# Optimization experiments

Hardware: AMD Instinct MI355X
Metric: run time of the kernel (lower is better)

Reference implementation:

```python
import jax, jax.numpy as jnp
import numpy as np
import math

H = 5       # attention heads
DK = 20     # attdim // H
ATT = 100   # attdim
LAYERS = 2
B, L, BERT_DIM = 32, 256, 768


def _layernorm(x, a, b, eps=1e-6):
    mean = x.mean(-1, keepdims=True)
    std = jnp.std(x, axis=-1, ddof=1, keepdims=True)  # torch.std is unbiased
    return a * (x - mean) / (std + eps) + b


def _forward(sequence_output, src_mask, aspect_mask, short_mask,
             ln_a, ln_b, Wxx_w, Wxx_b, q_w, q_b, k_w, k_b,
             dense_w, dense_b, bias_m, W_w, W_b, Wx_w, Wx_b, clf_w, clf_b):
    Bn, Ln, _ = sequence_output.shape
    x = _layernorm(sequence_output, ln_a, ln_b)
    g = x @ Wxx_w + Wxx_b                                  # [B,L,100]
    asp_wn = aspect_mask.sum(1, keepdims=True)             # [B,1]
    aspect = (g * aspect_mask[..., None]).sum(1) / asp_wn  # [B,100]

    q = (g @ q_w + q_b).reshape(Bn, Ln, H, DK).transpose(0, 2, 1, 3)  # [B,H,L,dk]
    k = (g @ k_w + k_b).reshape(Bn, Ln, H, DK).transpose(0, 2, 1, 3)
    # aspect is expanded identically across heads/positions before dense -> [B,dk]
    asp = aspect @ dense_w + dense_b                       # [B,dk]
    scores = jnp.einsum('bhid,bhjd->bhij', q, k) / math.sqrt(DK)
    asp_sc = jnp.tanh(jnp.einsum('bd,bhjd->bhj', asp, k) + bias_m[0])
    scores = scores + asp_sc[:, :, None, :]
    scores = jnp.where(src_mask[:, None, None, :] == 0, -1e9, scores)
    scores = scores + short_mask                           # [B,1,L,L] broadcast
    adj = jax.nn.softmax(scores, axis=-1)                  # [B,H,L,L]

    # edge-update linear split so the [B,L,L,205] concat is never materialized:
    # edge[b,i,j] = adj_perm[b,i,j] @ Wa + go[b,j] @ W1 + go[b,i] @ W2 + b
    Wa, W1, W2 = Wx_w[:H], Wx_w[H:H + ATT], Wx_w[H + ATT:]
    go = g
    for i in range(LAYERS):
        # expand+matmul+mean over heads == mean-head message passing
        Ax = jnp.einsum('bhij,bjd->bid', adj, go) / H
        go = jax.nn.relu(Ax @ W_w + W_b)
        if i < LAYERS - 1:  # last edge update is discarded by the original output
            edge = (jnp.einsum('bhij,hk->bijk', adj, Wa)
                    + (go @ W1)[:, None, :, :]
                    + (go @ W2)[:, :, None, :]
                    + Wx_b)
            adj = edge.transpose(0, 3, 1, 2)
    # original: node_outputs = F.relu(gcn_outputs) (aggregate_W result is overwritten)
    h = jax.nn.relu(go)
    out1 = (h * aspect_mask[..., None]).sum(1) / asp_wn    # [B,100]
    return out1 @ clf_w + clf_b                            # [B,3]


def setup_inputs() -> dict:
    key = jax.random.key(0)
    ks = jax.random.split(key, 24)
    f32 = jnp.float32
    p = lambda k, shape, s=0.05: jax.random.normal(k, shape, dtype=f32) * s
    src_mask = jax.random.randint(ks[0], (B, L), 0, 2, dtype=jnp.int32).at[:, 0].set(1)
    aspect_mask = jnp.zeros((B, L), f32).at[:, 4:8].set(1.0)  # aspect span tokens
    return {
        'sequence_output': jax.random.normal(ks[1], (B, L, BERT_DIM), dtype=f32),
        'src_mask': src_mask,
        'aspect_mask': aspect_mask,
        'short_mask': p(ks[2], (B, 1, L, L), 1.0),
        'ln_a': jnp.ones((BERT_DIM,), f32),
        'ln_b': jnp.zeros((BERT_DIM,), f32),
        'Wxx_w': p(ks[3], (BERT_DIM, ATT)), 'Wxx_b': p(ks[4], (ATT,)),
        'q_w': p(ks[5], (ATT, ATT)), 'q_b': p(ks[6], (ATT,)),
        'k_w': p(ks[7], (ATT, ATT)), 'k_b': p(ks[8], (ATT,)),
        'dense_w': p(ks[9], (ATT, DK)), 'dense_b': p(ks[10], (DK,)),
        'bias_m': p(ks[11], (1,)),
        'W_w': p(ks[12], (ATT, ATT)), 'W_b': p(ks[13], (ATT,)),
        'Wx_w': p(ks[14], (H + 2 * ATT, H)), 'Wx_b': p(ks[15], (H,)),
        'clf_w': p(ks[16], (ATT, 3)), 'clf_b': p(ks[17], (3,)),
    }


def reference(sequence_output, src_mask, aspect_mask, short_mask,
              ln_a, ln_b, Wxx_w, Wxx_b, q_w, q_b, k_w, k_b,
              dense_w, dense_b, bias_m, W_w, W_b, Wx_w, Wx_b, clf_w, clf_b):
    return _forward(sequence_output, src_mask, aspect_mask, short_mask,
                    ln_a, ln_b, Wxx_w, Wxx_b, q_w, q_b, k_w, k_b,
                    dense_w, dense_b, bias_m, W_w, W_b, Wx_w, Wx_b, clf_w, clf_b)
```

## Files before the change

### kernel.cpp

```cpp
#include <hip/hip_runtime.h>
#include <math.h>

constexpr int CL = 256;
constexpr int CD = 768;
constexpr int CATT = 100;
constexpr int CH = 5;
constexpr int CDK = 20;

__device__ __forceinline__ void fma4(float4& a, float s, const float4& w) {
    a.x = fmaf(s, w.x, a.x);
    a.y = fmaf(s, w.y, a.y);
    a.z = fmaf(s, w.z, a.z);
    a.w = fmaf(s, w.w, a.w);
}

__global__ __launch_bounds__(256) void k1_fused(
    const float* __restrict__ x, const float* __restrict__ ln_a,
    const float* __restrict__ ln_b, const float* __restrict__ Wxx_w,
    const float* __restrict__ Wxx_b, const float* __restrict__ q_w,
    const float* __restrict__ q_b, const float* __restrict__ k_w,
    const float* __restrict__ k_b, const float* __restrict__ amask,
    float* __restrict__ g, float* __restrict__ qt, float* __restrict__ ktb,
    float* __restrict__ aspect_raw)
{
    __shared__ float s_mean[16], s_rinv[16];
    __shared__ float s_xn[16 * 68];
    __shared__ float s_w[100 * 104];
    __shared__ float s_gt[16 * 100];

    const int t = threadIdx.x;
    const int r0 = blockIdx.x * 16;
    const int wid = t >> 6, lane = t & 63;

    for (int rr = wid * 4; rr < wid * 4 + 4; ++rr) {
        const float* xr = x + (size_t)(r0 + rr) * CD;
        float xv[12];
        float s = 0.f;
#pragma unroll
        for (int m = 0; m < 12; ++m) { xv[m] = xr[lane + 64 * m]; s += xv[m]; }
#pragma unroll
        for (int o = 32; o; o >>= 1) s += __shfl_xor(s, o);
        float mean = s * (1.0f / 768.0f);
        float sq = 0.f;
#pragma unroll
        for (int m = 0; m < 12; ++m) { float d = xv[m] - mean; sq = fmaf(d, d, sq); }
#pragma unroll
        for (int o = 32; o; o >>= 1) sq += __shfl_xor(sq, o);
        if (lane == 0) {
            s_mean[rr] = mean;
            s_rinv[rr] = 1.0f / (sqrtf(sq * (1.0f / 767.0f)) + 1e-6f);
        }
    }
    __syncthreads();

    const int cg = t % 25, rg = t / 25;
    const int c = cg * 4;
    float4 acc0 = make_float4(0.f, 0.f, 0.f, 0.f);
    float4 acc1 = make_float4(0.f, 0.f, 0.f, 0.f);

    for (int kt = 0; kt < 12; ++kt) {
#pragma unroll
        for (int m = 0; m < 4; ++m) {
            int idx = t + 256 * m;
            int row = idx >> 6, kk = idx & 63;
            int k = kt * 64 + kk;
            float v = x[(size_t)(r0 + row) * CD + k];
            s_xn[row * 68 + kk] = fmaf(ln_a[k], (v - s_mean[row]) * s_rinv[row], ln_b[k]);
        }
        const float4* wsrc = (const float4*)Wxx_w + (size_t)kt * 1600;
        for (int i = t; i < 1600; i += 256) {
            int row = i / 25, c4 = i % 25;
            *(float4*)&s_w[row * 104 + c4 * 4] = wsrc[i];
        }
        __syncthreads();
        if (t < 200) {
#pragma unroll 2
            for (int kk = 0; kk < 64; kk += 4) {
                float4 a0 = *(const float4*)&s_xn[(rg * 2 + 0) * 68 + kk];
                float4 a1 = *(const float4*)&s_xn[(rg * 2 + 1) * 68 + kk];
                float4 w0 = *(const float4*)&s_w[(kk + 0) * 104 + c];
                float4 w1 = *(const float4*)&s_w[(kk + 1) * 104 + c];
                float4 w2 = *(const float4*)&s_w[(kk + 2) * 104 + c];
                float4 w3 = *(const float4*)&s_w[(kk + 3) * 104 + c];
                fma4(acc0, a0.x, w0); fma4(acc0, a0.y, w1); fma4(acc0, a0.z, w2); fma4(acc0, a0.w, w3);
                fma4(acc1, a1.x, w0); fma4(acc1, a1.y, w1); fma4(acc1, a1.z, w2); fma4(acc1, a1.w, w3);
            }
        }
        __syncthreads();
    }
    if (t < 200) {
        float4 bias = *(const float4*)&Wxx_b[c];
        float4 rr0, rr1;
        rr0.x = acc0.x + bias.x; rr0.y = acc0.y + bias.y; rr0.z = acc0.z + bias.z; rr0.w = acc0.w + bias.w;
        rr1.x = acc1.x + bias.x; rr1.y = acc1.y + bias.y; rr1.z = acc1.z + bias.z; rr1.w = acc1.w + bias.w;
        float4 rv[2] = { rr0, rr1 };
#pragma unroll
        for (int q = 0; q < 2; ++q) {
            int row = r0 + rg * 2 + q;
            *(float4*)&g[(size_t)row * CATT + c] = rv[q];
            *(float4*)&s_gt[(rg * 2 + q) * 100 + c] = rv[q];
            float m = amask[row];
            if (m != 0.f) {
                int b = row >> 8;
                atomicAdd(&aspect_raw[b * CATT + c + 0], m * rv[q].x);
                atomicAdd(&aspect_raw[b * CATT + c + 1], m * rv[q].y);
                atomicAdd(&aspect_raw[b * CATT + c + 2], m * rv[q].z);
                atomicAdd(&aspect_raw[b * CATT + c + 3], m * rv[q].w);
            }
        }
    }
    __syncthreads();

    for (int pass = 0; pass < 2; ++pass) {
        const float4* ws4 = (const float4*)(pass ? k_w : q_w);
        for (int i = t; i < 2500; i += 256) {
            int row = i / 25, c4 = i % 25;
            *(float4*)&s_w[row * 104 + c4 * 4] = ws4[i];
        }
        __syncthreads();
        if (t < 200) {
            const float* bb = pass ? k_b : q_b;
            float* outp = pass ? ktb : qt;
            float4 b0 = make_float4(0.f, 0.f, 0.f, 0.f);
            float4 b1 = make_float4(0.f, 0.f, 0.f, 0.f);
#pragma unroll 2
            for (int k = 0; k < 100; k += 4) {
                float4 a0 = *(const float4*)&s_gt[(rg * 2 + 0) * 100 + k];
                float4 a1 = *(const float4*)&s_gt[(rg * 2 + 1) * 100 + k];
                float4 w0 = *(const float4*)&s_w[(k + 0) * 104 + c];
                float4 w1 = *(const float4*)&s_w[(k + 1) * 104 + c];
                float4 w2 = *(const float4*)&s_w[(k + 2) * 104 + c];
                float4 w3 = *(const float4*)&s_w[(k + 3) * 104 + c];
                fma4(b0, a0.x, w0); fma4(b0, a0.y, w1); fma4(b0, a0.z, w2); fma4(b0, a0.w, w3);
                fma4(b1, a1.x, w0); fma4(b1, a1.y, w1); fma4(b1, a1.z, w2); fma4(b1, a1.w, w3);
            }
            float4 bias = *(const float4*)&bb[c];
            b0.x += bias.x; b0.y += bias.y; b0.z += bias.z; b0.w += bias.w;
            b1.x += bias.x; b1.y += bias.y; b1.z += bias.z; b1.w += bias.w;
            const int h = c / CDK, d = c % CDK;
            float4 rv[2] = { b0, b1 };
#pragma unroll
            for (int q = 0; q < 2; ++q) {
                int row = r0 + rg * 2 + q;
                int bidx = row >> 8, l = row & 255;
                *(float4*)&outp[((size_t)(bidx * CH + h) * CL + l) * CDK + d] = rv[q];
            }
        }
        __syncthreads();
    }
}

__global__ __launch_bounds__(256) void k2_small(
    const float* __restrict__ aspect_raw, const float* __restrict__ amask,
    const float* __restrict__ dense_w, const float* __restrict__ dense_b,
    float* __restrict__ asp, float* __restrict__ aspwn)
{
    __shared__ float red[4];
    const int b = blockIdx.x, t = threadIdx.x;
    const int wid = t >> 6, lane = t & 63;
    float s = amask[b * CL + t];
#pragma unroll
    for (int o = 32; o; o >>= 1) s += __shfl_xor(s, o);
    if (lane == 0) red[wid] = s;
    __syncthreads();
    float wn = red[0] + red[1] + red[2] + red[3];
    if (t == 0) aspwn[b] = wn;
    if (t < 20) {
        float a = dense_b[t];
        float rwn = 1.f / wn;
        for (int d = 0; d < CATT; ++d)
            a = fmaf(aspect_raw[b * CATT + d] * rwn, dense_w[d * CDK + t], a);
        asp[b * CDK + t] = a;
    }
}

__global__ __launch_bounds__(256) void k45_attn_gcn0(
    const float* __restrict__ qt, const float* __restrict__ ktb,
    const float* __restrict__ asp, const float* __restrict__ bias_m,
    const int* __restrict__ src_mask, const float* __restrict__ shortm,
    const float* __restrict__ Wx_w, const float* __restrict__ g,
    const float* __restrict__ W_w, const float* __restrict__ W_b,
    float* __restrict__ adjW, float* __restrict__ go1,
    float* __restrict__ t1, float* __restrict__ t2, float* __restrict__ gW2S)
{
    constexpr int ICH = 16;
    __shared__ float s_adj[16 * 260];
    __shared__ float s_b[100 * 104];
    __shared__ float s_ax[16 * 108];
    __shared__ float s_q[ICH * CDK];
    __shared__ float s_red[ICH * 4];
    __shared__ float s_was[5];
    __shared__ float s_aspb[20];
    __shared__ float s_w1[100], s_w2[100];
    __shared__ float s_g1row[16];

    const int b = blockIdx.x >> 4, ic = blockIdx.x & 15;
    const int i0 = ic * 16;
    const int t = threadIdx.x, lane = t & 63, wid = t >> 6;
    const int j = t;

    if (t < 5) {
        float s = 0.f;
        for (int k2 = 0; k2 < 5; ++k2) s += Wx_w[t * 5 + k2];
        s_was[t] = s;
    }
    if (t < 20) s_aspb[t] = asp[b * CDK + t];
    if (t < 100) {
        float a = 0.f, c2 = 0.f;
#pragma unroll
        for (int h = 0; h < 5; ++h) {
            a += Wx_w[(5 + t) * 5 + h];
            c2 += Wx_w[(105 + t) * 5 + h];
        }
        s_w1[t] = a; s_w2[t] = c2;
    }

    const bool masked = (src_mask[b * CL + j] == 0);
    const float bm = bias_m[0];
    const float rs20 = 0.223606797749978969f;

    float sm[ICH];
#pragma unroll
    for (int ii = 0; ii < ICH; ++ii)
        sm[ii] = shortm[(size_t)(b * CL + i0 + ii) * CL + j];

    float accS[ICH], accW[ICH];
#pragma unroll
    for (int ii = 0; ii < ICH; ++ii) { accS[ii] = 0.f; accW[ii] = 0.f; }

    for (int h = 0; h < CH; ++h) {
        __syncthreads();
        {
            const size_t base = ((size_t)(b * CH + h) * CL + i0) * CDK;
            s_q[t] = qt[base + t];
            if (t < ICH * CDK - 256) s_q[256 + t] = qt[base + 256 + t];
        }
        float4 kr[5];
        const float* kp = ktb + ((size_t)(b * CH + h) * CL + j) * CDK;
#pragma unroll
        for (int m = 0; m < 5; ++m) kr[m] = *(const float4*)(kp + 4 * m);
        __syncthreads();

        const float was_h = s_was[h];
        float s = bm;
#pragma unroll
        for (int m = 0; m < 5; ++m) {
            s = fmaf(s_aspb[4 * m + 0], kr[m].x, s);
            s = fmaf(s_aspb[4 * m + 1], kr[m].y, s);
            s = fmaf(s_aspb[4 * m + 2], kr[m].z, s);
            s = fmaf(s_aspb[4 * m + 3], kr[m].w, s);
        }
        const float aspsc = tanhf(s);

        float pv[ICH];
#pragma unroll
        for (int ii = 0; ii < ICH; ++ii) {
            const float* qrow = &s_q[ii * CDK];
            float sc = 0.f;
#pragma unroll
            for (int m = 0; m < 5; ++m) {
                float4 q4 = *(const float4*)(qrow + 4 * m);
                sc = fmaf(q4.x, kr[m].x, sc);
                sc = fmaf(q4.y, kr[m].y, sc);
                sc = fmaf(q4.z, kr[m].z, sc);
                sc = fmaf(q4.w, kr[m].w, sc);
            }
            sc = fmaf(sc, rs20, aspsc) + sm[ii];
            float p = masked ? 0.f : __expf(sc);
            pv[ii] = p;
            float ssum = p;
#pragma unroll
            for (int o = 32; o; o >>= 1) ssum += __shfl_xor(ssum, o);
            if (lane == 0) s_red[ii * 4 + wid] = ssum;
        }
        __syncthreads();
#pragma unroll
        for (int ii = 0; ii < ICH; ++ii) {
            float tot = s_red[ii * 4 + 0] + s_red[ii * 4 + 1] +
                        s_red[ii * 4 + 2] + s_red[ii * 4 + 3];
            float pn = pv[ii] * __frcp_rn(tot);
            accS[ii] += pn;
            accW[ii] = fmaf(was_h, pn, accW[ii]);
        }
    }

#pragma unroll
    for (int ii = 0; ii < ICH; ++ii) {
        adjW[(size_t)(b * CL + i0 + ii) * CL + j] = accW[ii];
        s_adj[ii * 260 + j] = accS[ii];
    }
    __syncthreads();

    const int cg = t % 25, rg = t / 25;
    const int c = cg * 4;
    float4 acc0 = make_float4(0.f, 0.f, 0.f, 0.f);
    float4 acc1 = make_float4(0.f, 0.f, 0.f, 0.f);
    for (int jt = 0; jt < 4; ++jt) {
        const float4* src = (const float4*)g + (size_t)(b * CL + jt * 64) * 25;
        for (int i = t; i < 1600; i += 256) {
            int row = i / 25, c4 = i % 25;
            *(float4*)&s_b[row * 104 + c4 * 4] = src[i];
        }
        __syncthreads();
        if (t < 200) {
#pragma unroll 2
            for (int kk = 0; kk < 64; kk += 4) {
                float4 a0 = *(const float4*)&s_adj[(rg * 2 + 0) * 260 + jt * 64 + kk];
                float4 a1 = *(const float4*)&s_adj[(rg * 2 + 1) * 260 + jt * 64 + kk];
                float4 w0 = *(const float4*)&s_b[(kk + 0) * 104 + c];
                float4 w1 = *(const float4*)&s_b[(kk + 1) * 104 + c];
                float4 w2 = *(const float4*)&s_b[(kk + 2) * 104 + c];
                float4 w3 = *(const float4*)&s_b[(kk + 3) * 104 + c];
                fma4(acc0, a0.x, w0); fma4(acc0, a0.y, w1); fma4(acc0, a0.z, w2); fma4(acc0, a0.w, w3);
                fma4(acc1, a1.x, w0); fma4(acc1, a1.y, w1); fma4(acc1, a1.z, w2); fma4(acc1, a1.w, w3);
            }
        }
        __syncthreads();
    }
    if (t < 200) {
        float4 r;
        r.x = acc0.x * 0.2f; r.y = acc0.y * 0.2f; r.z = acc0.z * 0.2f; r.w = acc0.w * 0.2f;
        *(float4*)&s_ax[(rg * 2 + 0) * 108 + c] = r;
        r.x = acc1.x * 0.2f; r.y = acc1.y * 0.2f; r.z = acc1.z * 0.2f; r.w = acc1.w * 0.2f;
        *(float4*)&s_ax[(rg * 2 + 1) * 108 + c] = r;
    }
    {
        const float4* ws4 = (const float4*)W_w;
        for (int i = t; i < 2500; i += 256) {
            int row = i / 25, c4 = i % 25;
            *(float4*)&s_b[row * 104 + c4 * 4] = ws4[i];
        }
    }
    __syncthreads();

    float4 o0 = make_float4(0.f, 0.f, 0.f, 0.f);
    float4 o1 = make_float4(0.f, 0.f, 0.f, 0.f);
    if (t < 200) {
#pragma unroll 2
        for (int k = 0; k < 100; k += 4) {
            float4 a0 = *(const float4*)&s_ax[(rg * 2 + 0) * 108 + k];
            float4 a1 = *(const float4*)&s_ax[(rg * 2 + 1) * 108 + k];
            float4 w0 = *(const float4*)&s_b[(k + 0) * 104 + c];
            float4 w1 = *(const float4*)&s_b[(k + 1) * 104 + c];
            float4 w2 = *(const float4*)&s_b[(k + 2) * 104 + c];
            float4 w3 = *(const float4*)&s_b[(k + 3) * 104 + c];
            fma4(o0, a0.x, w0); fma4(o0, a0.y, w1); fma4(o0, a0.z, w2); fma4(o0, a0.w, w3);
            fma4(o1, a1.x, w0); fma4(o1, a1.y, w1); fma4(o1, a1.z, w2); fma4(o1, a1.w, w3);
        }
        float4 bias = *(const float4*)&W_b[c];
        o0.x = fmaxf(o0.x + bias.x, 0.f); o0.y = fmaxf(o0.y + bias.y, 0.f);
        o0.z = fmaxf(o0.z + bias.z, 0.f); o0.w = fmaxf(o0.w + bias.w, 0.f);
        o1.x = fmaxf(o1.x + bias.x, 0.f); o1.y = fmaxf(o1.y + bias.y, 0.f);
        o1.z = fmaxf(o1.z + bias.z, 0.f); o1.w = fmaxf(o1.w + bias.w, 0.f);
        *(float4*)&go1[(size_t)(b * CL + i0 + rg * 2 + 0) * CATT + c] = o0;
        *(float4*)&go1[(size_t)(b * CL + i0 + rg * 2 + 1) * CATT + c] = o1;
    }
    __syncthreads();

    float* s_go = s_adj;
    if (t < 200) {
        *(float4*)&s_go[(rg * 2 + 0) * 104 + c] = o0;
        *(float4*)&s_go[(rg * 2 + 1) * 104 + c] = o1;
    }
    __syncthreads();

    if (t < 128) {
        int r = t >> 3, seg = t & 7;
        int e0 = seg * 13, e1 = e0 + 13 < 100 ? e0 + 13 : 100;
        float a = 0.f, c2 = 0.f;
        for (int e = e0; e < e1; ++e) {
            float v = s_go[r * 104 + e];
            a = fmaf(v, s_w1[e], a);
            c2 = fmaf(v, s_w2[e], c2);
        }
        a += __shfl_xor(a, 1); a += __shfl_xor(a, 2); a += __shfl_xor(a, 4);
        c2 += __shfl_xor(c2, 1); c2 += __shfl_xor(c2, 2); c2 += __shfl_xor(c2, 4);
        if (seg == 0) {
            s_g1row[r] = a;
            gW2S[b * CL + i0 + r] = c2;
        }
    }
    __syncthreads();

    if (t < 100) {
        float a = 0.f, s2 = 0.f;
#pragma unroll
        for (int r = 0; r < 16; ++r) {
            float v = s_go[r * 104 + t];
            a = fmaf(s_g1row[r], v, a);
            s2 += v;
        }
        atomicAdd(&t1[b * CATT + t], a);
        atomicAdd(&t2[b * CATT + t], s2);
    }
}

__global__ __launch_bounds__(256) void k7_gcn1(
    const float* __restrict__ adjW, const float* __restrict__ go1,
    const float* __restrict__ W_w, const float* __restrict__ W_b,
    const float* __restrict__ t1, const float* __restrict__ t2,
    const float* __restrict__ gW2S, const float* __restrict__ Wx_b,
    const float* __restrict__ amask, float* __restrict__ out1_raw)
{
    __shared__ float s_adj[16 * 260];
    __shared__ float s_b[100 * 104];
    __shared__ float s_ax[16 * 108];
    const int b = blockIdx.x >> 4, ic = blockIdx.x & 15;
    const int i0 = ic * 16;
    const int t = threadIdx.x;

    {
        const float4* asrc = (const float4*)adjW + (size_t)(b * CL + i0) * 64;
        for (int i = t; i < 1024; i += 256) {
            int row = i >> 6, c4 = i & 63;
            *(float4*)&s_adj[row * 260 + c4 * 4] = asrc[i];
        }
    }
    __syncthreads();

    const int cg = t % 25, rg = t / 25;
    const int c = cg * 4;
    float4 acc0 = make_float4(0.f, 0.f, 0.f, 0.f);
    float4 acc1 = make_float4(0.f, 0.f, 0.f, 0.f);
    for (int jt = 0; jt < 4; ++jt) {
        const float4* src = (const float4*)go1 + (size_t)(b * CL + jt * 64) * 25;
        for (int i = t; i < 1600; i += 256) {
            int row = i / 25, c4 = i % 25;
            *(float4*)&s_b[row * 104 + c4 * 4] = src[i];
        }
        __syncthreads();
        if (t < 200) {
#pragma unroll 2
            for (int kk = 0; kk < 64; kk += 4) {
                float4 a0 = *(const float4*)&s_adj[(rg * 2 + 0) * 260 + jt * 64 + kk];
                float4 a1 = *(const float4*)&s_adj[(rg * 2 + 1) * 260 + jt * 64 + kk];
                float4 w0 = *(const float4*)&s_b[(kk + 0) * 104 + c];
                float4 w1 = *(const float4*)&s_b[(kk + 1) * 104 + c];
                float4 w2 = *(const float4*)&s_b[(kk + 2) * 104 + c];
                float4 w3 = *(const float4*)&s_b[(kk + 3) * 104 + c];
                fma4(acc0, a0.x, w0); fma4(acc0, a0.y, w1); fma4(acc0, a0.z, w2); fma4(acc0, a0.w, w3);
                fma4(acc1, a1.x, w0); fma4(acc1, a1.y, w1); fma4(acc1, a1.z, w2); fma4(acc1, a1.w, w3);
            }
        }
        __syncthreads();
    }
    if (t < 200) {
        float wxbs = Wx_b[0] + Wx_b[1] + Wx_b[2] + Wx_b[3] + Wx_b[4];
        float4 t1v = *(const float4*)&t1[b * CATT + c];
        float4 t2v = *(const float4*)&t2[b * CATT + c];
        float gw0 = gW2S[b * CL + i0 + rg * 2 + 0] + wxbs;
        float gw1 = gW2S[b * CL + i0 + rg * 2 + 1] + wxbs;
        float4 r;
        r.x = (acc0.x + t1v.x + gw0 * t2v.x) * 0.2f;
        r.y = (acc0.y + t1v.y + gw0 * t2v.y) * 0.2f;
        r.z = (acc0.z + t1v.z + gw0 * t2v.z) * 0.2f;
        r.w = (acc0.w + t1v.w + gw0 * t2v.w) * 0.2f;
        *(float4*)&s_ax[(rg * 2 + 0) * 108 + c] = r;
        r.x = (acc1.x + t1v.x + gw1 * t2v.x) * 0.2f;
        r.y = (acc1.y + t1v.y + gw1 * t2v.y) * 0.2f;
        r.z = (acc1.z + t1v.z + gw1 * t2v.z) * 0.2f;
        r.w = (acc1.w + t1v.w + gw1 * t2v.w) * 0.2f;
        *(float4*)&s_ax[(rg * 2 + 1) * 108 + c] = r;
    }
    {
        const float4* ws4 = (const float4*)W_w;
        for (int i = t; i < 2500; i += 256) {
            int row = i / 25, c4 = i % 25;
            *(float4*)&s_b[row * 104 + c4 * 4] = ws4[i];
        }
    }
    __syncthreads();

    if (t < 200) {
        float4 o0 = make_float4(0.f, 0.f, 0.f, 0.f);
        float4 o1 = make_float4(0.f, 0.f, 0.f, 0.f);
#pragma unroll 2
        for (int k = 0; k < 100; k += 4) {
            float4 a0 = *(const float4*)&s_ax[(rg * 2 + 0) * 108 + k];
            float4 a1 = *(const float4*)&s_ax[(rg * 2 + 1) * 108 + k];
            float4 w0 = *(const float4*)&s_b[(k + 0) * 104 + c];
            float4 w1 = *(const float4*)&s_b[(k + 1) * 104 + c];
            float4 w2 = *(const float4*)&s_b[(k + 2) * 104 + c];
            float4 w3 = *(const float4*)&s_b[(k + 3) * 104 + c];
            fma4(o0, a0.x, w0); fma4(o0, a0.y, w1); fma4(o0, a0.z, w2); fma4(o0, a0.w, w3);
            fma4(o1, a1.x, w0); fma4(o1, a1.y, w1); fma4(o1, a1.z, w2); fma4(o1, a1.w, w3);
        }
        float4 bias = *(const float4*)&W_b[c];
        o0.x = fmaxf(o0.x + bias.x, 0.f); o0.y = fmaxf(o0.y + bias.y, 0.f);
        o0.z = fmaxf(o0.z + bias.z, 0.f); o0.w = fmaxf(o0.w + bias.w, 0.f);
        o1.x = fmaxf(o1.x + bias.x, 0.f); o1.y = fmaxf(o1.y + bias.y, 0.f);
        o1.z = fmaxf(o1.z + bias.z, 0.f); o1.w = fmaxf(o1.w + bias.w, 0.f);
        float4 ov[2] = { o0, o1 };
#pragma unroll
        for (int q = 0; q < 2; ++q) {
            int row = b * CL + i0 + rg * 2 + q;
            float m = amask[row];
            if (m != 0.f) {
                atomicAdd(&out1_raw[b * CATT + c + 0], m * ov[q].x);
                atomicAdd(&out1_raw[b * CATT + c + 1], m * ov[q].y);
                atomicAdd(&out1_raw[b * CATT + c + 2], m * ov[q].z);
                atomicAdd(&out1_raw[b * CATT + c + 3], m * ov[q].w);
            }
        }
    }
}

__global__ __launch_bounds__(64) void k8_small(
    const float* __restrict__ out1_raw, const float* __restrict__ aspwn,
    const float* __restrict__ clf_w, const float* __restrict__ clf_b,
    float* __restrict__ out)
{
    const int b = blockIdx.x, t = threadIdx.x;
    if (t < 3) {
        float rwn = 1.f / aspwn[b];
        float a = clf_b[t];
        for (int d = 0; d < CATT; ++d)
            a = fmaf(out1_raw[b * CATT + d] * rwn, clf_w[d * 3 + t], a);
        out[b * 3 + t] = a;
    }
}

extern "C" void kernel_launch(void* const* d_in, const int* in_sizes, int n_in,
                              void* d_out, int out_size, void* d_ws, size_t ws_size,
                              hipStream_t stream) {
    const float* seq     = (const float*)d_in[0];
    const int*   srcm    = (const int*)d_in[1];
    const float* amask   = (const float*)d_in[2];
    const float* shortm  = (const float*)d_in[3];
    const float* ln_a    = (const float*)d_in[4];
    const float* ln_b    = (const float*)d_in[5];
    const float* Wxx_w   = (const float*)d_in[6];
    const float* Wxx_b   = (const float*)d_in[7];
    const float* q_w     = (const float*)d_in[8];
    const float* q_b     = (const float*)d_in[9];
    const float* k_w     = (const float*)d_in[10];
    const float* k_b     = (const float*)d_in[11];
    const float* dense_w = (const float*)d_in[12];
    const float* dense_b = (const float*)d_in[13];
    const float* bias_m  = (const float*)d_in[14];
    const float* W_w     = (const float*)d_in[15];
    const float* W_b     = (const float*)d_in[16];
    const float* Wx_w    = (const float*)d_in[17];
    const float* Wx_b    = (const float*)d_in[18];
    const float* clf_w   = (const float*)d_in[19];
    const float* clf_b   = (const float*)d_in[20];
    float* out = (float*)d_out;

    float* ws         = (float*)d_ws;
    float* g          = ws;
    float* qt         = g + 819200;
    float* ktb        = qt + 819200;
    float* go1        = ktb + 819200;
    float* adjW       = go1 + 819200;
    float* aspect_raw = adjW + 2097152;
    float* t1         = aspect_raw + 3200;
    float* t2         = t1 + 3200;
    float* out1_raw   = t2 + 3200;
    float* gW2S       = out1_raw + 3200;
    float* asp        = gW2S + 8192;
    float* aspwn      = asp + 640;

    hipMemsetAsync(aspect_raw, 0, 4 * 3200 * sizeof(float), stream);
    hipLaunchKernelGGL(k1_fused, dim3(512), dim3(256), 0, stream, seq, ln_a, ln_b,
                       Wxx_w, Wxx_b, q_w, q_b, k_w, k_b, amask, g, qt, ktb, aspect_raw);
    hipLaunchKernelGGL(k2_small, dim3(32), dim3(256), 0, stream,
                       aspect_raw, amask, dense_w, dense_b, asp, aspwn);
    hipLaunchKernelGGL(k45_attn_gcn0, dim3(512), dim3(256), 0, stream,
                       qt, ktb, asp, bias_m, srcm, shortm, Wx_w, g, W_w, W_b,
                       adjW, go1, t1, t2, gW2S);
    hipLaunchKernelGGL(k7_gcn1, dim3(512), dim3(256), 0, stream,
                       adjW, go1, W_w, W_b, t1, t2, gW2S, Wx_b, amask, out1_raw);
    hipLaunchKernelGGL(k8_small, dim3(32), dim3(64), 0, stream,
                       out1_raw, aspwn, clf_w, clf_b, out);
}
```

Measured before the change: 259.1 us.

## Double-buffer shared tiles with register prefetch and fold aspect kernel into attention

Adds register-staged prefetch with double-buffered shared-memory tiles in the LayerNorm/projection GEMM and both GCN aggregation loops. The next tile's global loads now overlap the current tile's FMAs, and one barrier per iteration is removed. The small aspect-projection kernel is merged into the attention kernel, and the aspect-mask sums are recomputed in place, which removes a launch. Per-head Q tiles are loaded once up front to drop per-head barriers. The cost is more shared memory and registers, which may lower occupancy, and the unpadded stride-100 layout may cause bank conflicts.

Result: slower. 280.0 us (+8.0%).

```diff
diff --git a/kernel.cpp b/kernel.cpp
--- a/kernel.cpp
+++ b/kernel.cpp
@@ -12,6 +12,19 @@
     a.y = fmaf(s, w.y, a.y);
     a.z = fmaf(s, w.z, a.z);
     a.w = fmaf(s, w.w, a.w);
+}
+
+struct WPref { float4 r[7]; };
+__device__ __forceinline__ void pref_load(WPref& p, const float4* __restrict__ src, int t) {
+#pragma unroll
+    for (int m = 0; m < 6; ++m) p.r[m] = src[t + 256 * m];
+    if (t < 64) p.r[6] = src[t + 1536];
+}
+__device__ __forceinline__ void pref_store(const WPref& p, float* dst, int t) {
+    float4* d4 = (float4*)dst;
+#pragma unroll
+    for (int m = 0; m < 6; ++m) d4[t + 256 * m] = p.r[m];
+    if (t < 64) d4[t + 1536] = p.r[6];
 }
 
 __global__ __launch_bounds__(256) void k1_fused(
@@ -23,10 +36,10 @@
     float* __restrict__ g, float* __restrict__ qt, float* __restrict__ ktb,
     float* __restrict__ aspect_raw)
 {
+    __shared__ float s_w[2][6400];
+    __shared__ float s_xn[2][16 * 68];
+    __shared__ float s_gt[16 * 100];
     __shared__ float s_mean[16], s_rinv[16];
-    __shared__ float s_xn[16 * 68];
-    __shared__ float s_w[100 * 104];
-    __shared__ float s_gt[16 * 100];
 
     const int t = threadIdx.x;
     const int r0 = blockIdx.x * 16;
@@ -51,49 +64,66 @@
             s_rinv[rr] = 1.0f / (sqrtf(sq * (1.0f / 767.0f)) + 1e-6f);
         }
     }
-    __syncthreads();
 
     const int cg = t % 25, rg = t / 25;
     const int c = cg * 4;
+    const int xrow = t >> 4, xc4 = t & 15;
+    const float* xrowp = x + (size_t)(r0 + xrow) * CD;
+
+    WPref wp;
+    pref_load(wp, (const float4*)Wxx_w, t);
+    float4 xp = *(const float4*)(xrowp + xc4 * 4);
+    float4 la = *(const float4*)(ln_a + xc4 * 4);
+    float4 lb = *(const float4*)(ln_b + xc4 * 4);
+
+    __syncthreads();
+
     float4 acc0 = make_float4(0.f, 0.f, 0.f, 0.f);
     float4 acc1 = make_float4(0.f, 0.f, 0.f, 0.f);
 
     for (int kt = 0; kt < 12; ++kt) {
-#pragma unroll
-        for (int m = 0; m < 4; ++m) {
-            int idx = t + 256 * m;
-            int row = idx >> 6, kk = idx & 63;
-            int k = kt * 64 + kk;
-            float v = x[(size_t)(r0 + row) * CD + k];
-            s_xn[row * 68 + kk] = fmaf(ln_a[k], (v - s_mean[row]) * s_rinv[row], ln_b[k]);
-        }
-        const float4* wsrc = (const float4*)Wxx_w + (size_t)kt * 1600;
-        for (int i = t; i < 1600; i += 256) {
-            int row = i / 25, c4 = i % 25;
-            *(float4*)&s_w[row * 104 + c4 * 4] = wsrc[i];
+        float* wbuf = s_w[kt & 1];
+        float* xbuf = s_xn[kt & 1];
+        {
+            float mean = s_mean[xrow], rinv = s_rinv[xrow];
+            float4 v;
+            v.x = fmaf(la.x, (xp.x - mean) * rinv, lb.x);
+            v.y = fmaf(la.y, (xp.y - mean) * rinv, lb.y);
+            v.z = fmaf(la.z, (xp.z - mean) * rinv, lb.z);
+            v.w = fmaf(la.w, (xp.w - mean) * rinv, lb.w);
+            *(float4*)&xbuf[xrow * 68 + xc4 * 4] = v;
+            pref_store(wp, wbuf, t);
+        }
+        if (kt < 11) {
+            pref_load(wp, (const float4*)Wxx_w + (size_t)(kt + 1) * 1600, t);
+            int kb = (kt + 1) * 64 + xc4 * 4;
+            xp = *(const float4*)(xrowp + kb);
+            la = *(const float4*)(ln_a + kb);
+            lb = *(const float4*)(ln_b + kb);
         }
         __syncthreads();
         if (t < 200) {
 #pragma unroll 2
             for (int kk = 0; kk < 64; kk += 4) {
-                float4 a0 = *(const float4*)&s_xn[(rg * 2 + 0) * 68 + kk];
-                float4 a1 = *(const float4*)&s_xn[(rg * 2 + 1) * 68 + kk];
-                float4 w0 = *(const float4*)&s_w[(kk + 0) * 104 + c];
-                float4 w1 = *(const float4*)&s_w[(kk + 1) * 104 + c];
-                float4 w2 = *(const float4*)&s_w[(kk + 2) * 104 + c];
-                float4 w3 = *(const float4*)&s_w[(kk + 3) * 104 + c];
+                float4 a0 = *(const float4*)&xbuf[(rg * 2 + 0) * 68 + kk];
+                float4 a1 = *(const float4*)&xbuf[(rg * 2 + 1) * 68 + kk];
+                float4 w0 = *(const float4*)&wbuf[(kk + 0) * 100 + c];
+                float4 w1 = *(const float4*)&wbuf[(kk + 1) * 100 + c];
+                float4 w2 = *(const float4*)&wbuf[(kk + 2) * 100 + c];
+                float4 w3 = *(const float4*)&wbuf[(kk + 3) * 100 + c];
                 fma4(acc0, a0.x, w0); fma4(acc0, a0.y, w1); fma4(acc0, a0.z, w2); fma4(acc0, a0.w, w3);
                 fma4(acc1, a1.x, w0); fma4(acc1, a1.y, w1); fma4(acc1, a1.z, w2); fma4(acc1, a1.w, w3);
             }
         }
-        __syncthreads();
-    }
+    }
+    __syncthreads();
+
     if (t < 200) {
         float4 bias = *(const float4*)&Wxx_b[c];
-        float4 rr0, rr1;
-        rr0.x = acc0.x + bias.x; rr0.y = acc0.y + bias.y; rr0.z = acc0.z + bias.z; rr0.w = acc0.w + bias.w;
-        rr1.x = acc1.x + bias.x; rr1.y = acc1.y + bias.y; rr1.z = acc1.z + bias.z; rr1.w = acc1.w + bias.w;
-        float4 rv[2] = { rr0, rr1 };
+        float4 rv0, rv1;
+        rv0.x = acc0.x + bias.x; rv0.y = acc0.y + bias.y; rv0.z = acc0.z + bias.z; rv0.w = acc0.w + bias.w;
+        rv1.x = acc1.x + bias.x; rv1.y = acc1.y + bias.y; rv1.z = acc1.z + bias.z; rv1.w = acc1.w + bias.w;
+        float4 rv[2] = { rv0, rv1 };
 #pragma unroll
         for (int q = 0; q < 2; ++q) {
             int row = r0 + rg * 2 + q;
@@ -109,14 +139,11 @@
             }
         }
     }
-    __syncthreads();
-
+
+    float* swf = &s_w[0][0];
     for (int pass = 0; pass < 2; ++pass) {
         const float4* ws4 = (const float4*)(pass ? k_w : q_w);
-        for (int i = t; i < 2500; i += 256) {
-            int row = i / 25, c4 = i % 25;
-            *(float4*)&s_w[row * 104 + c4 * 4] = ws4[i];
-        }
+        for (int i = t; i < 2500; i += 256) ((float4*)swf)[i] = ws4[i];
         __syncthreads();
         if (t < 200) {
             const float* bb = pass ? k_b : q_b;
@@ -127,10 +154,10 @@
             for (int k = 0; k < 100; k += 4) {
                 float4 a0 = *(const float4*)&s_gt[(rg * 2 + 0) * 100 + k];
                 float4 a1 = *(const float4*)&s_gt[(rg * 2 + 1) * 100 + k];
-                float4 w0 = *(const float4*)&s_w[(k + 0) * 104 + c];
-                float4 w1 = *(const float4*)&s_w[(k + 1) * 104 + c];
-                float4 w2 = *(const float4*)&s_w[(k + 2) * 104 + c];
-                float4 w3 = *(const float4*)&s_w[(k + 3) * 104 + c];
+                float4 w0 = *(const float4*)&swf[(k + 0) * 100 + c];
+                float4 w1 = *(const float4*)&swf[(k + 1) * 100 + c];
+                float4 w2 = *(const float4*)&swf[(k + 2) * 100 + c];
+                float4 w3 = *(const float4*)&swf[(k + 3) * 100 + c];
                 fma4(b0, a0.x, w0); fma4(b0, a0.y, w1); fma4(b0, a0.z, w2); fma4(b0, a0.w, w3);
                 fma4(b1, a1.x, w0); fma4(b1, a1.y, w1); fma4(b1, a1.z, w2); fma4(b1, a1.w, w3);
             }
@@ -150,52 +177,29 @@
     }
 }
 
-__global__ __launch_bounds__(256) void k2_small(
+__global__ __launch_bounds__(256) void k45_attn_gcn0(
+    const float* __restrict__ qt, const float* __restrict__ ktb,
     const float* __restrict__ aspect_raw, const float* __restrict__ amask,
     const float* __restrict__ dense_w, const float* __restrict__ dense_b,
-    float* __restrict__ asp, float* __restrict__ aspwn)
-{
-    __shared__ float red[4];
-    const int b = blockIdx.x, t = threadIdx.x;
-    const int wid = t >> 6, lane = t & 63;
-    float s = amask[b * CL + t];
-#pragma unroll
-    for (int o = 32; o; o >>= 1) s += __shfl_xor(s, o);
-    if (lane == 0) red[wid] = s;
-    __syncthreads();
-    float wn = red[0] + red[1] + red[2] + red[3];
-    if (t == 0) aspwn[b] = wn;
-    if (t < 20) {
-        float a = dense_b[t];
-        float rwn = 1.f / wn;
-        for (int d = 0; d < CATT; ++d)
-            a = fmaf(aspect_raw[b * CATT + d] * rwn, dense_w[d * CDK + t], a);
-        asp[b * CDK + t] = a;
-    }
-}
-
-__global__ __launch_bounds__(256) void k45_attn_gcn0(
-    const float* __restrict__ qt, const float* __restrict__ ktb,
-    const float* __restrict__ asp, const float* __restrict__ bias_m,
-    const int* __restrict__ src_mask, const float* __restrict__ shortm,
-    const float* __restrict__ Wx_w, const float* __restrict__ g,
-    const float* __restrict__ W_w, const float* __restrict__ W_b,
-    float* __restrict__ adjW, float* __restrict__ go1,
-    float* __restrict__ t1, float* __restrict__ t2, float* __restrict__ gW2S)
+    const float* __restrict__ bias_m, const int* __restrict__ src_mask,
+    const float* __restrict__ shortm, const float* __restrict__ Wx_w,
+    const float* __restrict__ g, const float* __restrict__ W_w,
+    const float* __restrict__ W_b, float* __restrict__ adjW,
+    float* __restrict__ go1, float* __restrict__ t1, float* __restrict__ t2,
+    float* __restrict__ gW2S)
 {
     constexpr int ICH = 16;
-    __shared__ float s_adj[16 * 260];
-    __shared__ float s_b[100 * 104];
-    __shared__ float s_ax[16 * 108];
-    __shared__ float s_q[ICH * CDK];
-    __shared__ float s_red[ICH * 4];
+    __shared__ float s_pool[16 * 260];
+    __shared__ float s_w[2][6400];
+    __shared__ float s_q[CH * 320];
+    __shared__ float s_red[CH][64];
     __shared__ float s_was[5];
     __shared__ float s_aspb[20];
     __shared__ float s_w1[100], s_w2[100];
     __shared__ float s_g1row[16];
 
     const int b = blockIdx.x >> 4, ic = blockIdx.x & 15;
-    const int i0 = ic * 16;
+    const int i0 = ic * ICH;
     const int t = threadIdx.x, lane = t & 63, wid = t >> 6;
     const int j = t;
 
@@ -204,7 +208,6 @@
         for (int k2 = 0; k2 < 5; ++k2) s += Wx_w[t * 5 + k2];
         s_was[t] = s;
     }
-    if (t < 20) s_aspb[t] = asp[b * CDK + t];
     if (t < 100) {
         float a = 0.f, c2 = 0.f;
 #pragma unroll
@@ -214,6 +217,26 @@
         }
         s_w1[t] = a; s_w2[t] = c2;
     }
+    float wn = 0.f;
+    if (t < 64) {
+        float4 mv = ((const float4*)amask)[b * 64 + t];
+        wn = mv.x + mv.y + mv.z + mv.w;
+#pragma unroll
+        for (int o = 32; o; o >>= 1) wn += __shfl_xor(wn, o);
+    }
+    if (t < 20) {
+        float a = 0.f;
+        for (int d = 0; d < CATT; ++d)
+            a = fmaf(aspect_raw[b * CATT + d], dense_w[d * CDK + t], a);
+        s_aspb[t] = a / wn + dense_b[t];
+    }
+    {
+        const float* qbase = qt + (size_t)b * CH * CL * CDK + (size_t)i0 * CDK;
+        for (int i = t; i < CH * 320; i += 256) {
+            int h = i / 320, r = i % 320;
+            s_q[i] = qbase[(size_t)h * CL * CDK + r];
+        }
+    }
 
     const bool masked = (src_mask[b * CL + j] == 0);
     const float bm = bias_m[0];
@@ -228,19 +251,13 @@
 #pragma unroll
     for (int ii = 0; ii < ICH; ++ii) { accS[ii] = 0.f; accW[ii] = 0.f; }
 
+    __syncthreads();
+
     for (int h = 0; h < CH; ++h) {
-        __syncthreads();
-        {
-            const size_t base = ((size_t)(b * CH + h) * CL + i0) * CDK;
-            s_q[t] = qt[base + t];
-            if (t < ICH * CDK - 256) s_q[256 + t] = qt[base + 256 + t];
-        }
         float4 kr[5];
         const float* kp = ktb + ((size_t)(b * CH + h) * CL + j) * CDK;
 #pragma unroll
         for (int m = 0; m < 5; ++m) kr[m] = *(const float4*)(kp + 4 * m);
-        __syncthreads();
-
         const float was_h = s_was[h];
         float s = bm;
 #pragma unroll
@@ -255,7 +272,7 @@
         float pv[ICH];
 #pragma unroll
         for (int ii = 0; ii < ICH; ++ii) {
-            const float* qrow = &s_q[ii * CDK];
+            const float* qrow = &s_q[h * 320 + ii * CDK];
             float sc = 0.f;
 #pragma unroll
             for (int m = 0; m < 5; ++m) {
@@ -271,13 +288,13 @@
             float ssum = p;
 #pragma unroll
             for (int o = 32; o; o >>= 1) ssum += __shfl_xor(ssum, o);
-            if (lane == 0) s_red[ii * 4 + wid] = ssum;
+            if (lane == 0) s_red[h][ii * 4 + wid] = ssum;
         }
         __syncthreads();
 #pragma unroll
         for (int ii = 0; ii < ICH; ++ii) {
-            float tot = s_red[ii * 4 + 0] + s_red[ii * 4 + 1] +
-                        s_red[ii * 4 + 2] + s_red[ii * 4 + 3];
+            float tot = s_red[h][ii * 4 + 0] + s_red[h][ii * 4 + 1] +
+                        s_red[h][ii * 4 + 2] + s_red[h][ii * 4 + 3];
             float pn = pv[ii] * __frcp_rn(tot);
             accS[ii] += pn;
             accW[ii] = fmaf(was_h, pn, accW[ii]);
@@ -287,36 +304,39 @@
 #pragma unroll
     for (int ii = 0; ii < ICH; ++ii) {
         adjW[(size_t)(b * CL + i0 + ii) * CL + j] = accW[ii];
-        s_adj[ii * 260 + j] = accS[ii];
-    }
-    __syncthreads();
+        s_pool[ii * 260 + j] = accS[ii];
+    }
 
     const int cg = t % 25, rg = t / 25;
     const int c = cg * 4;
+    WPref wp;
+    pref_load(wp, (const float4*)g + (size_t)b * CL * 25, t);
+
     float4 acc0 = make_float4(0.f, 0.f, 0.f, 0.f);
     float4 acc1 = make_float4(0.f, 0.f, 0.f, 0.f);
     for (int jt = 0; jt < 4; ++jt) {
-        const float4* src = (const float4*)g + (size_t)(b * CL + jt * 64) * 25;
-        for (int i = t; i < 1600; i += 256) {
-            int row = i / 25, c4 = i % 25;
-            *(float4*)&s_b[row * 104 + c4 * 4] = src[i];
-        }
+        float* wbuf = s_w[jt & 1];
+        pref_store(wp, wbuf, t);
+        if (jt < 3)
+            pref_load(wp, (const float4*)g + (size_t)(b * CL + (jt + 1) * 64) * 25, t);
         __syncthreads();
         if (t < 200) {
 #pragma unroll 2
             for (int kk = 0; kk < 64; kk += 4) {
-                float4 a0 = *(const float4*)&s_adj[(rg * 2 + 0) * 260 + jt * 64 + kk];
-                float4 a1 = *(const float4*)&s_adj[(rg * 2 + 1) * 260 + jt * 64 + kk];
-                float4 w0 = *(const float4*)&s_b[(kk + 0) * 104 + c];
-                float4 w1 = *(const float4*)&s_b[(kk + 1) * 104 + c];
-                float4 w2 = *(const float4*)&s_b[(kk + 2) * 104 + c];
-                float4 w3 = *(const float4*)&s_b[(kk + 3) * 104 + c];
+                float4 a0 = *(const float4*)&s_pool[(rg * 2 + 0) * 260 + jt * 64 + kk];
+                float4 a1 = *(const float4*)&s_pool[(rg * 2 + 1) * 260 + jt * 64 + kk];
+                float4 w0 = *(const float4*)&wbuf[(kk + 0) * 100 + c];
+                float4 w1 = *(const float4*)&wbuf[(kk + 1) * 100 + c];
+                float4 w2 = *(const float4*)&wbuf[(kk + 2) * 100 + c];
+                float4 w3 = *(const float4*)&wbuf[(kk + 3) * 100 + c];
                 fma4(acc0, a0.x, w0); fma4(acc0, a0.y, w1); fma4(acc0, a0.z, w2); fma4(acc0, a0.w, w3);
                 fma4(acc1, a1.x, w0); fma4(acc1, a1.y, w1); fma4(acc1, a1.z, w2); fma4(acc1, a1.w, w3);
             }
         }
-        __syncthreads();
-    }
+    }
+    __syncthreads();
+
+    float* s_ax = s_pool;
     if (t < 200) {
         float4 r;
         r.x = acc0.x * 0.2f; r.y = acc0.y * 0.2f; r.z = acc0.z * 0.2f; r.w = acc0.w * 0.2f;
@@ -324,12 +344,10 @@
         r.x = acc1.x * 0.2f; r.y = acc1.y * 0.2f; r.z = acc1.z * 0.2f; r.w = acc1.w * 0.2f;
         *(float4*)&s_ax[(rg * 2 + 1) * 108 + c] = r;
     }
+    float* swf = &s_w[0][0];
     {
         const float4* ws4 = (const float4*)W_w;
-        for (int i = t; i < 2500; i += 256) {
-            int row = i / 25, c4 = i % 25;
-            *(float4*)&s_b[row * 104 + c4 * 4] = ws4[i];
-        }
+        for (int i = t; i < 2500; i += 256) ((float4*)swf)[i] = ws4[i];
     }
     __syncthreads();
 
@@ -340,10 +358,10 @@
         for (int k = 0; k < 100; k += 4) {
             float4 a0 = *(const float4*)&s_ax[(rg * 2 + 0) * 108 + k];
             float4 a1 = *(const float4*)&s_ax[(rg * 2 + 1) * 108 + k];
-            float4 w0 = *(const float4*)&s_b[(k + 0) * 104 + c];
-            float4 w1 = *(const float4*)&s_b[(k + 1) * 104 + c];
-            float4 w2 = *(const float4*)&s_b[(k + 2) * 104 + c];
-            float4 w3 = *(const float4*)&s_b[(k + 3) * 104 + c];
+            float4 w0 = *(const float4*)&swf[(k + 0) * 100 + c];
+            float4 w1 = *(const float4*)&swf[(k + 1) * 100 + c];
+            float4 w2 = *(const float4*)&swf[(k + 2) * 100 + c];
+            float4 w3 = *(const float4*)&swf[(k + 3) * 100 + c];
             fma4(o0, a0.x, w0); fma4(o0, a0.y, w1); fma4(o0, a0.z, w2); fma4(o0, a0.w, w3);
             fma4(o1, a1.x, w0); fma4(o1, a1.y, w1); fma4(o1, a1.z, w2); fma4(o1, a1.w, w3);
         }
@@ -355,9 +373,7 @@
         *(float4*)&go1[(size_t)(b * CL + i0 + rg * 2 + 0) * CATT + c] = o0;
         *(float4*)&go1[(size_t)(b * CL + i0 + rg * 2 + 1) * CATT + c] = o1;
     }
-    __syncthreads();
-
-    float* s_go = s_adj;
+    float* s_go = s_pool + 1728;
     if (t < 200) {
         *(float4*)&s_go[(rg * 2 + 0) * 104 + c] = o0;
         *(float4*)&s_go[(rg * 2 + 1) * 104 + c] = o1;
@@ -402,48 +418,52 @@
     const float* __restrict__ gW2S, const float* __restrict__ Wx_b,
     const float* __restrict__ amask, float* __restrict__ out1_raw)
 {
-    __shared__ float s_adj[16 * 260];
-    __shared__ float s_b[100 * 104];
-    __shared__ float s_ax[16 * 108];
+    __shared__ float s_pool[16 * 260];
+    __shared__ float s_w[2][6400];
     const int b = blockIdx.x >> 4, ic = blockIdx.x & 15;
     const int i0 = ic * 16;
     const int t = threadIdx.x;
 
     {
         const float4* asrc = (const float4*)adjW + (size_t)(b * CL + i0) * 64;
-        for (int i = t; i < 1024; i += 256) {
+#pragma unroll
+        for (int m = 0; m < 4; ++m) {
+            int i = t + 256 * m;
             int row = i >> 6, c4 = i & 63;
-            *(float4*)&s_adj[row * 260 + c4 * 4] = asrc[i];
-        }
-    }
-    __syncthreads();
+            *(float4*)&s_pool[row * 260 + c4 * 4] = asrc[i];
+        }
+    }
 
     const int cg = t % 25, rg = t / 25;
     const int c = cg * 4;
+    WPref wp;
+    pref_load(wp, (const float4*)go1 + (size_t)b * CL * 25, t);
+
     float4 acc0 = make_float4(0.f, 0.f, 0.f, 0.f);
     float4 acc1 = make_float4(0.f, 0.f, 0.f, 0.f);
     for (int jt = 0; jt < 4; ++jt) {
-        const float4* src = (const float4*)go1 + (size_t)(b * CL + jt * 64) * 25;
-        for (int i = t; i < 1600; i += 256) {
-            int row = i / 25, c4 = i % 25;
-            *(float4*)&s_b[row * 104 + c4 * 4] = src[i];
-        }
+        float* wbuf = s_w[jt & 1];
+        pref_store(wp, wbuf, t);
+        if (jt < 3)
+            pref_load(wp, (const float4*)go1 + (size_t)(b * CL + (jt + 1) * 64) * 25, t);
         __syncthreads();
         if (t < 200) {
 #pragma unroll 2
             for (int kk = 0; kk < 64; kk += 4) {
-                float4 a0 = *(const float4*)&s_adj[(rg * 2 + 0) * 260 + jt * 64 + kk];
-                float4 a1 = *(const float4*)&s_adj[(rg * 2 + 1) * 260 + jt * 64 + kk];
-                float4 w0 = *(const float4*)&s_b[(kk + 0) * 104 + c];
-                float4 w1 = *(const float4*)&s_b[(kk + 1) * 104 + c];
-                float4 w2 = *(const float4*)&s_b[(kk + 2) * 104 + c];
-                float4 w3 = *(const float4*)&s_b[(kk + 3) * 104 + c];
+                float4 a0 = *(const float4*)&s_pool[(rg * 2 + 0) * 260 + jt * 64 + kk];
+                float4 a1 = *(const float4*)&s_pool[(rg * 2 + 1) * 260 + jt * 64 + kk];
+                float4 w0 = *(const float4*)&wbuf[(kk + 0) * 100 + c];
+                float4 w1 = *(const float4*)&wbuf[(kk + 1) * 100 + c];
+                float4 w2 = *(const float4*)&wbuf[(kk + 2) * 100 + c];
+                float4 w3 = *(const float4*)&wbuf[(kk + 3) * 100 + c];
                 fma4(acc0, a0.x, w0); fma4(acc0, a0.y, w1); fma4(acc0, a0.z, w2); fma4(acc0, a0.w, w3);
                 fma4(acc1, a1.x, w0); fma4(acc1, a1.y, w1); fma4(acc1, a1.z, w2); fma4(acc1, a1.w, w3);
             }
         }
-        __syncthreads();
-    }
+    }
+    __syncthreads();
+
+    float* s_ax = s_pool;
     if (t < 200) {
         float wxbs = Wx_b[0] + Wx_b[1] + Wx_b[2] + Wx_b[3] + Wx_b[4];
         float4 t1v = *(const float4*)&t1[b * CATT + c];
@@ -462,12 +482,10 @@
         r.w = (acc1.w + t1v.w + gw1 * t2v.w) * 0.2f;
         *(float4*)&s_ax[(rg * 2 + 1) * 108 + c] = r;
     }
+    float* swf = &s_w[0][0];
     {
         const float4* ws4 = (const float4*)W_w;
-        for (int i = t; i < 2500; i += 256) {
-            int row = i / 25, c4 = i % 25;
-            *(float4*)&s_b[row * 104 + c4 * 4] = ws4[i];
-        }
+        for (int i = t; i < 2500; i += 256) ((float4*)swf)[i] = ws4[i];
     }
     __syncthreads();
 
@@ -478,10 +496,10 @@
         for (int k = 0; k < 100; k += 4) {
             float4 a0 = *(const float4*)&s_ax[(rg * 2 + 0) * 108 + k];
             float4 a1 = *(const float4*)&s_ax[(rg * 2 + 1) * 108 + k];
-            float4 w0 = *(const float4*)&s_b[(k + 0) * 104 + c];
-            float4 w1 = *(const float4*)&s_b[(k + 1) * 104 + c];
-            float4 w2 = *(const float4*)&s_b[(k + 2) * 104 + c];
-            float4 w3 = *(const float4*)&s_b[(k + 3) * 104 + c];
+            float4 w0 = *(const float4*)&swf[(k + 0) * 100 + c];
+            float4 w1 = *(const float4*)&swf[(k + 1) * 100 + c];
+            float4 w2 = *(const float4*)&swf[(k + 2) * 100 + c];
+            float4 w3 = *(const float4*)&swf[(k + 3) * 100 + c];
             fma4(o0, a0.x, w0); fma4(o0, a0.y, w1); fma4(o0, a0.z, w2); fma4(o0, a0.w, w3);
             fma4(o1, a1.x, w0); fma4(o1, a1.y, w1); fma4(o1, a1.z, w2); fma4(o1, a1.w, w3);
         }
@@ -506,13 +524,17 @@
 }
 
 __global__ __launch_bounds__(64) void k8_small(
-    const float* __restrict__ out1_raw, const float* __restrict__ aspwn,
+    const float* __restrict__ out1_raw, const float* __restrict__ amask,
     const float* __restrict__ clf_w, const float* __restrict__ clf_b,
     float* __restrict__ out)
 {
     const int b = blockIdx.x, t = threadIdx.x;
+    float4 mv = ((const float4*)amask)[b * 64 + t];
+    float wn = mv.x + mv.y + mv.z + mv.w;
+#pragma unroll
+    for (int o = 32; o; o >>= 1) wn += __shfl_xor(wn, o);
     if (t < 3) {
-        float rwn = 1.f / aspwn[b];
+        float rwn = 1.f / wn;
         float a = clf_b[t];
         for (int d = 0; d < CATT; ++d)
             a = fmaf(out1_raw[b * CATT + d] * rwn, clf_w[d * 3 + t], a);
@@ -557,19 +579,15 @@
     float* t2         = t1 + 3200;
     float* out1_raw   = t2 + 3200;
     float* gW2S       = out1_raw + 3200;
-    float* asp        = gW2S + 8192;
-    float* aspwn      = asp + 640;
 
     hipMemsetAsync(aspect_raw, 0, 4 * 3200 * sizeof(float), stream);
     hipLaunchKernelGGL(k1_fused, dim3(512), dim3(256), 0, stream, seq, ln_a, ln_b,
                        Wxx_w, Wxx_b, q_w, q_b, k_w, k_b, amask, g, qt, ktb, aspect_raw);
-    hipLaunchKernelGGL(k2_small, dim3(32), dim3(256), 0, stream,
-                       aspect_raw, amask, dense_w, dense_b, asp, aspwn);
     hipLaunchKernelGGL(k45_attn_gcn0, dim3(512), dim3(256), 0, stream,
-                       qt, ktb, asp, bias_m, srcm, shortm, Wx_w, g, W_w, W_b,
-                       adjW, go1, t1, t2, gW2S);
+                       qt, ktb, aspect_raw, amask, dense_w, dense_b, bias_m, srcm,
+                       shortm, Wx_w, g, W_w, W_b, adjW, go1, t1, t2, gW2S);
     hipLaunchKernelGGL(k7_gcn1, dim3(512), dim3(256), 0, stream,
                        adjW, go1, W_w, W_b, t1, t2, gW2S, Wx_b, amask, out1_raw);
     hipLaunchKernelGGL(k8_small, dim3(32), dim3(64), 0, stream,
-                       out1_raw, aspwn, clf_w, clf_b, out);
-}
+                       out1_raw, amask, clf_w, clf_b, out);
+}
```
